# Kernel tuning notes

Hardware: AMD Instinct MI355X
Metric: run time of the kernel (lower is better)

The kernel has to match this reference:

```python
import jax, jax.numpy as jnp
import numpy as np

B, N, C = 32, 577, 768
H = 12
D = C // H
HID = 4 * C
EPS = 1e-5


def setup_inputs() -> dict:
    key = jax.random.key(0)
    ks = jax.random.split(key, 12)
    s = 0.02
    return {
        "x": jax.random.normal(ks[0], (B, N, C), dtype=jnp.float32),
        "ln1_g": jnp.ones((C,), jnp.float32),
        "ln1_b": jnp.zeros((C,), jnp.float32),
        "qkv_w": jax.random.normal(ks[1], (C, 3 * C), jnp.float32) * s,
        "qkv_b": jnp.zeros((3 * C,), jnp.float32),
        "proj_w": jax.random.normal(ks[2], (C, C), jnp.float32) * s,
        "proj_b": jnp.zeros((C,), jnp.float32),
        "ln2_g": jnp.ones((C,), jnp.float32),
        "ln2_b": jnp.zeros((C,), jnp.float32),
        "fc1_w": jax.random.normal(ks[3], (C, HID), jnp.float32) * s,
        "fc1_b": jnp.zeros((HID,), jnp.float32),
        "fc2_w": jax.random.normal(ks[4], (HID, C), jnp.float32) * s,
        "fc2_b": jnp.zeros((C,), jnp.float32),
    }


def _layernorm(x, g, b):
    mu = jnp.mean(x, axis=-1, keepdims=True)
    var = jnp.mean(jnp.square(x - mu), axis=-1, keepdims=True)
    return (x - mu) * jax.lax.rsqrt(var + EPS) * g + b


def reference(x, ln1_g, ln1_b, qkv_w, qkv_b, proj_w, proj_b,
              ln2_g, ln2_b, fc1_w, fc1_b, fc2_w, fc2_b):
    b, n, c = x.shape
    # --- MSA branch ---
    h = _layernorm(x, ln1_g, ln1_b)
    qkv = h @ qkv_w + qkv_b                      # [b, n, 3c]
    qkv = qkv.reshape(b, n, 3, H, D).transpose(2, 0, 3, 1, 4)  # [3, b, h, n, d]
    q, k, v = qkv[0], qkv[1], qkv[2]
    scale = D ** -0.5
    attn = jnp.einsum('bhqd,bhkd->bhqk', q, k) * scale
    attn = jax.nn.softmax(attn, axis=-1)
    o = jnp.einsum('bhqk,bhkd->bhqd', attn, v)   # [b, h, n, d]
    o = o.transpose(0, 2, 1, 3).reshape(b, n, c)
    o = o @ proj_w + proj_b
    x = x + o
    # --- MLP branch ---
    h = _layernorm(x, ln2_g, ln2_b)
    h = jax.nn.gelu(h @ fc1_w + fc1_b, approximate=False)  # torch nn.GELU = exact erf
    h = h @ fc2_w + fc2_b
    return x + h
```

## Files before the change

### kernel.cpp

```cpp
#include <hip/hip_runtime.h>

typedef unsigned short u16;
typedef short short8 __attribute__((ext_vector_type(8)));
typedef float f32x4 __attribute__((ext_vector_type(4)));

#define MM 18464
#define NTOK 577

__device__ __forceinline__ u16 f2bf(float f) {
    unsigned u = __builtin_bit_cast(unsigned, f);
    u += 0x7fffu + ((u >> 16) & 1u);
    return (u16)(u >> 16);
}

__device__ __forceinline__ void gload16(const void* g, void* lds) {
    __builtin_amdgcn_global_load_lds(
        (const __attribute__((address_space(1))) unsigned*)g,
        (__attribute__((address_space(3))) unsigned*)lds,
        16, 0, 0);
}

__device__ __forceinline__ int2 xcd_swz(int gx, int gy) {
    const int nwg = gx * gy;
    const int flat = blockIdx.x + blockIdx.y * gx;
    const int q = nwg >> 3, r = nwg & 7;
    const int xcd = flat & 7, lid = flat >> 3;
    const int w = (xcd < r ? xcd * (q + 1) : r * (q + 1) + (xcd - r) * q) + lid;
    int2 o; o.x = w % gx; o.y = w / gx; return o;
}

__global__ __launch_bounds__(256) void convT(const float* __restrict__ src,
                                             u16* __restrict__ dst, int K, int N) {
    __shared__ float tile[32][33];
    const int k0 = blockIdx.x * 32, n0 = blockIdx.y * 32;
    const int tx = threadIdx.x & 31, ty = threadIdx.x >> 5;
#pragma unroll
    for (int i = 0; i < 32; i += 8)
        tile[ty + i][tx] = src[(size_t)(k0 + ty + i) * N + n0 + tx];
    __syncthreads();
#pragma unroll
    for (int i = 0; i < 32; i += 8)
        dst[(size_t)(n0 + ty + i) * K + k0 + tx] = f2bf(tile[tx][ty + i]);
}

__global__ __launch_bounds__(192) void ln_k(const float* __restrict__ x,
                                            const float* __restrict__ g,
                                            const float* __restrict__ bt,
                                            u16* __restrict__ out) {
    const int row = blockIdx.x, t = threadIdx.x;
    const float4 v = reinterpret_cast<const float4*>(x + (size_t)row * 768)[t];
    float s = v.x + v.y + v.z + v.w;
    float s2 = v.x * v.x + v.y * v.y + v.z * v.z + v.w * v.w;
#pragma unroll
    for (int off = 32; off > 0; off >>= 1) {
        s += __shfl_down(s, off);
        s2 += __shfl_down(s2, off);
    }
    __shared__ float red[6];
    if ((t & 63) == 0) { red[t >> 6] = s; red[3 + (t >> 6)] = s2; }
    __syncthreads();
    const float S = red[0] + red[1] + red[2];
    const float S2 = red[3] + red[4] + red[5];
    const float mu = S * (1.f / 768.f);
    const float var = S2 * (1.f / 768.f) - mu * mu;
    const float rs = rsqrtf(var + 1e-5f);
    const float4 gg = reinterpret_cast<const float4*>(g)[t];
    const float4 bb = reinterpret_cast<const float4*>(bt)[t];
    ushort4 r;
    r.x = f2bf((v.x - mu) * rs * gg.x + bb.x);
    r.y = f2bf((v.y - mu) * rs * gg.y + bb.y);
    r.z = f2bf((v.z - mu) * rs * gg.z + bb.z);
    r.w = f2bf((v.w - mu) * rs * gg.w + bb.w);
    reinterpret_cast<ushort4*>(out + (size_t)row * 768)[t] = r;
}

template <int MODE>
__global__ __launch_bounds__(256) void gemm_k(const u16* __restrict__ A,
                                              const u16* __restrict__ BT,
                                              const float* __restrict__ bias,
                                              const float* __restrict__ resid,
                                              void* __restrict__ outp,
                                              int M, int N, int K) {
    __shared__ u16 As[2][128 * 32];
    __shared__ u16 Bs[2][128 * 32];
    const int t = threadIdx.x;
    const int wid = t >> 6, lane = t & 63;
    const int l15 = lane & 15, lg = lane >> 4;
    const int2 sw = xcd_swz(gridDim.x, gridDim.y);
    const int m0 = sw.x * 128, n0 = sw.y * 128;
    const int wr = wid >> 1, wc = wid & 1;

    f32x4 acc[4][4] = {};

    const int srow = t >> 2;
    const int sk = (t & 3) * 8;
    const size_t a0 = (size_t)min(m0 + srow, M - 1) * K + sk;
    const size_t a1 = (size_t)min(m0 + srow + 64, M - 1) * K + sk;
    const size_t b0 = (size_t)(n0 + srow) * K + sk;
    const size_t b1 = (size_t)(n0 + srow + 64) * K + sk;
    const int wo = wid * 512;

    auto stage = [&](int buf, int k0) {
        gload16(A + a0 + k0, &As[buf][wo]);
        gload16(A + a1 + k0, &As[buf][wo + 2048]);
        gload16(BT + b0 + k0, &Bs[buf][wo]);
        gload16(BT + b1 + k0, &Bs[buf][wo + 2048]);
    };
    auto compute = [&](int buf) {
        short8 af[4], bfr[4];
#pragma unroll
        for (int fr = 0; fr < 4; ++fr)
            af[fr] = *(const short8*)&As[buf][(wr * 64 + fr * 16 + l15) * 32 + lg * 8];
#pragma unroll
        for (int fc = 0; fc < 4; ++fc)
            bfr[fc] = *(const short8*)&Bs[buf][(wc * 64 + fc * 16 + l15) * 32 + lg * 8];
#pragma unroll
        for (int fr = 0; fr < 4; ++fr)
#pragma unroll
            for (int fc = 0; fc < 4; ++fc)
                acc[fr][fc] = __builtin_amdgcn_mfma_f32_16x16x32_bf16(
                    af[fr], bfr[fc], acc[fr][fc], 0, 0, 0);
    };

    stage(0, 0);
    __syncthreads();
    int cur = 0;
    const int nk = K >> 5;
    for (int kt = 1; kt < nk; ++kt) {
        stage(cur ^ 1, kt * 32);
        compute(cur);
        __syncthreads();
        cur ^= 1;
    }
    compute(cur);

    float bcol[4];
#pragma unroll
    for (int fc = 0; fc < 4; ++fc) bcol[fc] = bias[n0 + wc * 64 + fc * 16 + l15];
#pragma unroll
    for (int fr = 0; fr < 4; ++fr) {
#pragma unroll
        for (int reg = 0; reg < 4; ++reg) {
            const int row = m0 + wr * 64 + fr * 16 + lg * 4 + reg;
            if (row < M) {
#pragma unroll
                for (int fc = 0; fc < 4; ++fc) {
                    const int col = n0 + wc * 64 + fc * 16 + l15;
                    float v = acc[fr][fc][reg] + bcol[fc];
                    if (MODE == 2) v = 0.5f * v * (1.0f + erff(v * 0.70710678118f));
                    if (MODE == 1 || MODE == 3) v += resid[(size_t)row * N + col];
                    if (MODE == 0 || MODE == 2)
                        ((u16*)outp)[(size_t)row * N + col] = f2bf(v);
                    else
                        ((float*)outp)[(size_t)row * N + col] = v;
                }
            }
        }
    }
}

__global__ __launch_bounds__(256) void attn_k(const u16* __restrict__ qkv,
                                              u16* __restrict__ o) {
    const int2 sw = xcd_swz(10, 384);
    const int qt = sw.x;
    const int bh = sw.y;
    const int b = bh / 12, h = bh % 12;
    const int t = threadIdx.x, wid = t >> 6, lane = t & 63;
    const int l15 = lane & 15, lg = lane >> 4;
    const size_t base = ((size_t)b * NTOK) * 2304 + (size_t)h * 64;

    __shared__ u16 Ks[64 * 64], VT[64 * 64], Ps[64 * 64];

    int qrow = qt * 64 + wid * 16 + l15;
    qrow = min(qrow, NTOK - 1);
    const u16* Qp = qkv + base + (size_t)qrow * 2304 + lg * 8;
    const short8 qf0 = *(const short8*)(Qp);
    const short8 qf1 = *(const short8*)(Qp + 32);

    f32x4 oacc[4] = {};
    float m_run[4], l_run[4];
#pragma unroll
    for (int j = 0; j < 4; ++j) { m_run[j] = -1e30f; l_run[j] = 0.f; }

    const int srow = t >> 3;
    const int cchunk = t & 7;
    const int ksd = (cchunk ^ (srow & 7)) * 8;
    u16* ldsK = Ks + wid * 512;
    const int vs0 = ((srow >> 3) ^ cchunk) * 8 + (srow & 7);
    const int vs1 = (((srow >> 3) + 4) ^ cchunk) * 8 + (srow & 7);

    for (int kt = 0; kt < 10; ++kt) {
        const int n0t = kt * 64;
        const int r0 = min(n0t + srow, NTOK - 1);
        const int r1 = min(n0t + srow + 32, NTOK - 1);
        gload16(qkv + base + 768 + (size_t)r0 * 2304 + ksd, ldsK);
        gload16(qkv + base + 768 + (size_t)r1 * 2304 + ksd, ldsK + 2048);
        const short8 v0 = *(const short8*)(qkv + base + 1536 + (size_t)r0 * 2304 + cchunk * 8);
        const short8 v1 = *(const short8*)(qkv + base + 1536 + (size_t)r1 * 2304 + cchunk * 8);
#pragma unroll
        for (int j = 0; j < 8; ++j) {
            VT[(cchunk * 8 + j) * 64 + vs0] = (u16)v0[j];
            VT[(cchunk * 8 + j) * 64 + vs1] = (u16)v1[j];
        }
        __syncthreads();

        f32x4 s[4];
#pragma unroll
        for (int fc = 0; fc < 4; ++fc) {
            const int krow = fc * 16 + l15;
            const short8 kf0 = *(const short8*)&Ks[krow * 64 + ((lg ^ (krow & 7)) * 8)];
            const short8 kf1 = *(const short8*)&Ks[krow * 64 + (((lg + 4) ^ (krow & 7)) * 8)];
            f32x4 a_ = {};
            a_ = __builtin_amdgcn_mfma_f32_16x16x32_bf16(qf0, kf0, a_, 0, 0, 0);
            a_ = __builtin_amdgcn_mfma_f32_16x16x32_bf16(qf1, kf1, a_, 0, 0, 0);
            s[fc] = a_;
        }
#pragma unroll
        for (int fc = 0; fc < 4; ++fc) {
            const bool valid = (n0t + fc * 16 + l15) < NTOK;
#pragma unroll
            for (int j = 0; j < 4; ++j)
                s[fc][j] = valid ? s[fc][j] * 0.125f : -1e30f;
        }
        float mt[4];
#pragma unroll
        for (int j = 0; j < 4; ++j)
            mt[j] = fmaxf(fmaxf(s[0][j], s[1][j]), fmaxf(s[2][j], s[3][j]));
#pragma unroll
        for (int off = 1; off < 16; off <<= 1)
#pragma unroll
            for (int j = 0; j < 4; ++j) mt[j] = fmaxf(mt[j], __shfl_xor(mt[j], off));
        float mn[4], alpha[4];
#pragma unroll
        for (int j = 0; j < 4; ++j) {
            mn[j] = fmaxf(m_run[j], mt[j]);
            alpha[j] = __expf(m_run[j] - mn[j]);
            m_run[j] = mn[j];
        }
        float lsum[4] = {0.f, 0.f, 0.f, 0.f};
#pragma unroll
        for (int fc = 0; fc < 4; ++fc)
#pragma unroll
            for (int j = 0; j < 4; ++j) {
                const float p = __expf(s[fc][j] - mn[j]);
                s[fc][j] = p;
                lsum[j] += p;
            }
#pragma unroll
        for (int off = 1; off < 16; off <<= 1)
#pragma unroll
            for (int j = 0; j < 4; ++j) lsum[j] += __shfl_xor(lsum[j], off);
#pragma unroll
        for (int j = 0; j < 4; ++j) l_run[j] = l_run[j] * alpha[j] + lsum[j];
#pragma unroll
        for (int fc = 0; fc < 4; ++fc)
#pragma unroll
            for (int j = 0; j < 4; ++j) oacc[fc][j] *= alpha[j];

#pragma unroll
        for (int fc = 0; fc < 4; ++fc)
#pragma unroll
            for (int j = 0; j < 4; ++j) {
                const int q = wid * 16 + lg * 4 + j;
                Ps[q * 64 + (((fc * 2 + (l15 >> 3)) ^ (q & 7)) * 8) + (l15 & 7)] =
                    f2bf(s[fc][j]);
            }
        asm volatile("s_waitcnt lgkmcnt(0)" ::: "memory");

#pragma unroll
        for (int c = 0; c < 2; ++c) {
            const short8 pf = *(const short8*)
                &Ps[(wid * 16 + l15) * 64 + (((c * 4 + lg) ^ (l15 & 7)) * 8)];
#pragma unroll
            for (int fc = 0; fc < 4; ++fc) {
                const short8 vf = *(const short8*)
                    &VT[(fc * 16 + l15) * 64 +
                        (((c * 4 + lg) ^ (fc * 2 + (l15 >> 3))) * 8)];
                oacc[fc] = __builtin_amdgcn_mfma_f32_16x16x32_bf16(pf, vf, oacc[fc], 0, 0, 0);
            }
        }
        __syncthreads();
    }

#pragma unroll
    for (int j = 0; j < 4; ++j) {
        const int row = qt * 64 + wid * 16 + lg * 4 + j;
        if (row < NTOK) {
            const float inv = 1.0f / l_run[j];
#pragma unroll
            for (int fc = 0; fc < 4; ++fc)
                o[((size_t)(b * NTOK + row)) * 768 + h * 64 + fc * 16 + l15] =
                    f2bf(oacc[fc][j] * inv);
        }
    }
}

extern "C" void kernel_launch(void* const* d_in, const int* in_sizes, int n_in,
                              void* d_out, int out_size, void* d_ws, size_t ws_size,
                              hipStream_t stream) {
    const float* x      = (const float*)d_in[0];
    const float* ln1_g  = (const float*)d_in[1];
    const float* ln1_b  = (const float*)d_in[2];
    const float* qkv_w  = (const float*)d_in[3];
    const float* qkv_b  = (const float*)d_in[4];
    const float* proj_w = (const float*)d_in[5];
    const float* proj_b = (const float*)d_in[6];
    const float* ln2_g  = (const float*)d_in[7];
    const float* ln2_b  = (const float*)d_in[8];
    const float* fc1_w  = (const float*)d_in[9];
    const float* fc1_b  = (const float*)d_in[10];
    const float* fc2_w  = (const float*)d_in[11];
    const float* fc2_b  = (const float*)d_in[12];
    float* out = (float*)d_out;

    char* ws = (char*)d_ws;
    size_t off = 0;
    u16* WQ  = (u16*)(ws + off); off += (size_t)2304 * 768 * 2;
    u16* WP  = (u16*)(ws + off); off += (size_t)768 * 768 * 2;
    u16* W1  = (u16*)(ws + off); off += (size_t)3072 * 768 * 2;
    u16* W2  = (u16*)(ws + off); off += (size_t)768 * 3072 * 2;
    u16* LN1 = (u16*)(ws + off); off += (size_t)MM * 768 * 2;
    u16* QKV = (u16*)(ws + off); off += (size_t)MM * 2304 * 2;
    u16* OB  = (u16*)(ws + off); off += (size_t)MM * 768 * 2;
    float* X1 = (float*)(ws + off); off += (size_t)MM * 768 * 4;
    u16* LN2 = (u16*)(ws + off); off += (size_t)MM * 768 * 2;
    u16* HID = LN1;

    convT<<<dim3(24, 72), 256, 0, stream>>>(qkv_w, WQ, 768, 2304);
    convT<<<dim3(24, 24), 256, 0, stream>>>(proj_w, WP, 768, 768);
    convT<<<dim3(24, 96), 256, 0, stream>>>(fc1_w, W1, 768, 3072);
    convT<<<dim3(96, 24), 256, 0, stream>>>(fc2_w, W2, 3072, 768);

    ln_k<<<MM, 192, 0, stream>>>(x, ln1_g, ln1_b, LN1);
    gemm_k<0><<<dim3(145, 18), 256, 0, stream>>>(LN1, WQ, qkv_b, nullptr, QKV,
                                                 MM, 2304, 768);
    attn_k<<<dim3(10, 384), 256, 0, stream>>>(QKV, OB);
    gemm_k<1><<<dim3(145, 6), 256, 0, stream>>>(OB, WP, proj_b, x, X1,
                                                MM, 768, 768);
    ln_k<<<MM, 192, 0, stream>>>(X1, ln2_g, ln2_b, LN2);
    gemm_k<2><<<dim3(145, 24), 256, 0, stream>>>(LN2, W1, fc1_b, nullptr, HID,
                                                 MM, 3072, 768);
    gemm_k<3><<<dim3(145, 6), 256, 0, stream>>>(HID, W2, fc2_b, X1, out,
                                                MM, 768, 3072);
}
```

Measured before the change: 849.2 us.

## Move GEMMs to 256x256 tiles with swizzled LDS and a two-stage async pipeline

Rewrites the shared GEMM kernel to use 512-thread blocks computing 256x256 output tiles with a K-step of 64, so each staged byte is reused across more MFMAs. LDS tiles are XOR-swizzled to avoid bank conflicts on fragment reads. A two-deep global_load_lds prefetch is gated by explicit vmcnt waits and barriers, and the MFMA block is wrapped in s_setprio. The cost is 128 KB of LDS per block, which allows one block per CU. The narrow proj and fc2 GEMMs now launch fewer blocks than there are CUs, and the M tail wastes more work.

```diff
diff --git a/kernel.cpp b/kernel.cpp
--- a/kernel.cpp
+++ b/kernel.cpp
@@ -20,12 +20,14 @@
         16, 0, 0);
 }
 
-__device__ __forceinline__ int2 xcd_swz(int gx, int gy) {
-    const int nwg = gx * gy;
-    const int flat = blockIdx.x + blockIdx.y * gx;
+__device__ __forceinline__ int xcd_map(int flat, int nwg) {
     const int q = nwg >> 3, r = nwg & 7;
     const int xcd = flat & 7, lid = flat >> 3;
-    const int w = (xcd < r ? xcd * (q + 1) : r * (q + 1) + (xcd - r) * q) + lid;
+    return (xcd < r ? xcd * (q + 1) : r * (q + 1) + (xcd - r) * q) + lid;
+}
+
+__device__ __forceinline__ int2 xcd_swz2(int gx, int gy) {
+    const int w = xcd_map(blockIdx.x + blockIdx.y * gx, gx * gy);
     int2 o; o.x = w % gx; o.y = w / gx; return o;
 }
 
@@ -75,78 +77,93 @@
 }
 
 template <int MODE>
-__global__ __launch_bounds__(256) void gemm_k(const u16* __restrict__ A,
-                                              const u16* __restrict__ BT,
-                                              const float* __restrict__ bias,
-                                              const float* __restrict__ resid,
-                                              void* __restrict__ outp,
-                                              int M, int N, int K) {
-    __shared__ u16 As[2][128 * 32];
-    __shared__ u16 Bs[2][128 * 32];
+__global__ __launch_bounds__(512, 2) void gemm_k(const u16* __restrict__ A,
+                                                 const u16* __restrict__ BT,
+                                                 const float* __restrict__ bias,
+                                                 const float* __restrict__ resid,
+                                                 void* __restrict__ outp,
+                                                 int M, int N, int K, int mt) {
+    __shared__ u16 smem[4][256 * 64];
     const int t = threadIdx.x;
     const int wid = t >> 6, lane = t & 63;
     const int l15 = lane & 15, lg = lane >> 4;
-    const int2 sw = xcd_swz(gridDim.x, gridDim.y);
-    const int m0 = sw.x * 128, n0 = sw.y * 128;
-    const int wr = wid >> 1, wc = wid & 1;
-
-    f32x4 acc[4][4] = {};
-
-    const int srow = t >> 2;
-    const int sk = (t & 3) * 8;
-    const size_t a0 = (size_t)min(m0 + srow, M - 1) * K + sk;
-    const size_t a1 = (size_t)min(m0 + srow + 64, M - 1) * K + sk;
-    const size_t b0 = (size_t)(n0 + srow) * K + sk;
-    const size_t b1 = (size_t)(n0 + srow + 64) * K + sk;
-    const int wo = wid * 512;
+    const int wr = wid >> 2, wc = wid & 3;
+
+    const int w = xcd_map(blockIdx.x, gridDim.x);
+    const int m0 = (w % mt) * 256, n0 = (w / mt) * 256;
+
+    f32x4 acc[8][4] = {};
+    const int NT = K >> 6;
 
     auto stage = [&](int buf, int k0) {
-        gload16(A + a0 + k0, &As[buf][wo]);
-        gload16(A + a1 + k0, &As[buf][wo + 2048]);
-        gload16(BT + b0 + k0, &Bs[buf][wo]);
-        gload16(BT + b1 + k0, &Bs[buf][wo + 2048]);
+        u16* Ad = smem[buf * 2];
+        u16* Bd = smem[buf * 2 + 1];
+#pragma unroll
+        for (int i = 0; i < 4; ++i) {
+            const int slot = i * 512 + t;
+            const int r = slot >> 3, sl = slot & 7;
+            const int cs = (sl ^ (r & 7)) << 3;
+            const size_t dofs = (size_t)(i * 512 + (t & ~63)) * 8;
+            gload16(A + (size_t)min(m0 + r, M - 1) * K + k0 + cs, Ad + dofs);
+            gload16(BT + (size_t)(n0 + r) * K + k0 + cs, Bd + dofs);
+        }
     };
+
     auto compute = [&](int buf) {
-        short8 af[4], bfr[4];
-#pragma unroll
-        for (int fr = 0; fr < 4; ++fr)
-            af[fr] = *(const short8*)&As[buf][(wr * 64 + fr * 16 + l15) * 32 + lg * 8];
-#pragma unroll
-        for (int fc = 0; fc < 4; ++fc)
-            bfr[fc] = *(const short8*)&Bs[buf][(wc * 64 + fc * 16 + l15) * 32 + lg * 8];
-#pragma unroll
-        for (int fr = 0; fr < 4; ++fr)
-#pragma unroll
-            for (int fc = 0; fc < 4; ++fc)
-                acc[fr][fc] = __builtin_amdgcn_mfma_f32_16x16x32_bf16(
-                    af[fr], bfr[fc], acc[fr][fc], 0, 0, 0);
+        const u16* Ab = smem[buf * 2];
+        const u16* Bb = smem[buf * 2 + 1];
+#pragma unroll
+        for (int half = 0; half < 2; ++half) {
+            short8 af[8], bf4[4];
+#pragma unroll
+            for (int mf = 0; mf < 8; ++mf) {
+                const int r = wr * 128 + mf * 16 + l15;
+                af[mf] = *(const short8*)&Ab[r * 64 + (((half * 4 + lg) ^ (l15 & 7)) << 3)];
+            }
+#pragma unroll
+            for (int nf = 0; nf < 4; ++nf) {
+                const int r = wc * 64 + nf * 16 + l15;
+                bf4[nf] = *(const short8*)&Bb[r * 64 + (((half * 4 + lg) ^ (l15 & 7)) << 3)];
+            }
+            __builtin_amdgcn_s_setprio(1);
+#pragma unroll
+            for (int mf = 0; mf < 8; ++mf)
+#pragma unroll
+                for (int nf = 0; nf < 4; ++nf)
+                    acc[mf][nf] = __builtin_amdgcn_mfma_f32_16x16x32_bf16(
+                        af[mf], bf4[nf], acc[mf][nf], 0, 0, 0);
+            __builtin_amdgcn_s_setprio(0);
+        }
     };
 
     stage(0, 0);
-    __syncthreads();
-    int cur = 0;
-    const int nk = K >> 5;
-    for (int kt = 1; kt < nk; ++kt) {
-        stage(cur ^ 1, kt * 32);
-        compute(cur);
-        __syncthreads();
-        cur ^= 1;
-    }
-    compute(cur);
+    stage(1, 64);
+    for (int tt = 0; tt < NT; ++tt) {
+        if (tt < NT - 1) asm volatile("s_waitcnt vmcnt(8)" ::: "memory");
+        else             asm volatile("s_waitcnt vmcnt(0)" ::: "memory");
+        __builtin_amdgcn_s_barrier();
+        __builtin_amdgcn_sched_barrier(0);
+        compute(tt & 1);
+        __builtin_amdgcn_sched_barrier(0);
+        asm volatile("s_waitcnt lgkmcnt(0)" ::: "memory");
+        __builtin_amdgcn_s_barrier();
+        __builtin_amdgcn_sched_barrier(0);
+        if (tt + 2 < NT) stage(tt & 1, (tt + 2) << 6);
+    }
 
     float bcol[4];
 #pragma unroll
-    for (int fc = 0; fc < 4; ++fc) bcol[fc] = bias[n0 + wc * 64 + fc * 16 + l15];
-#pragma unroll
-    for (int fr = 0; fr < 4; ++fr) {
+    for (int nf = 0; nf < 4; ++nf) bcol[nf] = bias[n0 + wc * 64 + nf * 16 + l15];
+#pragma unroll
+    for (int mf = 0; mf < 8; ++mf) {
 #pragma unroll
         for (int reg = 0; reg < 4; ++reg) {
-            const int row = m0 + wr * 64 + fr * 16 + lg * 4 + reg;
+            const int row = m0 + wr * 128 + mf * 16 + lg * 4 + reg;
             if (row < M) {
 #pragma unroll
-                for (int fc = 0; fc < 4; ++fc) {
-                    const int col = n0 + wc * 64 + fc * 16 + l15;
-                    float v = acc[fr][fc][reg] + bcol[fc];
+                for (int nf = 0; nf < 4; ++nf) {
+                    const int col = n0 + wc * 64 + nf * 16 + l15;
+                    float v = acc[mf][nf][reg] + bcol[nf];
                     if (MODE == 2) v = 0.5f * v * (1.0f + erff(v * 0.70710678118f));
                     if (MODE == 1 || MODE == 3) v += resid[(size_t)row * N + col];
                     if (MODE == 0 || MODE == 2)
@@ -161,7 +178,7 @@
 
 __global__ __launch_bounds__(256) void attn_k(const u16* __restrict__ qkv,
                                               u16* __restrict__ o) {
-    const int2 sw = xcd_swz(10, 384);
+    const int2 sw = xcd_swz2(10, 384);
     const int qt = sw.x;
     const int bh = sw.y;
     const int b = bh / 12, h = bh % 12;
@@ -222,18 +239,18 @@
             for (int j = 0; j < 4; ++j)
                 s[fc][j] = valid ? s[fc][j] * 0.125f : -1e30f;
         }
-        float mt[4];
+        float mt_[4];
 #pragma unroll
         for (int j = 0; j < 4; ++j)
-            mt[j] = fmaxf(fmaxf(s[0][j], s[1][j]), fmaxf(s[2][j], s[3][j]));
+            mt_[j] = fmaxf(fmaxf(s[0][j], s[1][j]), fmaxf(s[2][j], s[3][j]));
 #pragma unroll
         for (int off = 1; off < 16; off <<= 1)
 #pragma unroll
-            for (int j = 0; j < 4; ++j) mt[j] = fmaxf(mt[j], __shfl_xor(mt[j], off));
+            for (int j = 0; j < 4; ++j) mt_[j] = fmaxf(mt_[j], __shfl_xor(mt_[j], off));
         float mn[4], alpha[4];
 #pragma unroll
         for (int j = 0; j < 4; ++j) {
-            mn[j] = fmaxf(m_run[j], mt[j]);
+            mn[j] = fmaxf(m_run[j], mt_[j]);
             alpha[j] = __expf(m_run[j] - mn[j]);
             m_run[j] = mn[j];
         }
@@ -331,15 +348,16 @@
     convT<<<dim3(24, 96), 256, 0, stream>>>(fc1_w, W1, 768, 3072);
     convT<<<dim3(96, 24), 256, 0, stream>>>(fc2_w, W2, 3072, 768);
 
+    const int mt = (MM + 255) / 256;
     ln_k<<<MM, 192, 0, stream>>>(x, ln1_g, ln1_b, LN1);
-    gemm_k<0><<<dim3(145, 18), 256, 0, stream>>>(LN1, WQ, qkv_b, nullptr, QKV,
-                                                 MM, 2304, 768);
+    gemm_k<0><<<mt * 9, 512, 0, stream>>>(LN1, WQ, qkv_b, nullptr, QKV,
+                                          MM, 2304, 768, mt);
     attn_k<<<dim3(10, 384), 256, 0, stream>>>(QKV, OB);
-    gemm_k<1><<<dim3(145, 6), 256, 0, stream>>>(OB, WP, proj_b, x, X1,
-                                                MM, 768, 768);
+    gemm_k<1><<<mt * 3, 512, 0, stream>>>(OB, WP, proj_b, x, X1,
+                                          MM, 768, 768, mt);
     ln_k<<<MM, 192, 0, stream>>>(X1, ln2_g, ln2_b, LN2);
-    gemm_k<2><<<dim3(145, 24), 256, 0, stream>>>(LN2, W1, fc1_b, nullptr, HID,
-                                                 MM, 3072, 768);
-    gemm_k<3><<<dim3(145, 6), 256, 0, stream>>>(HID, W2, fc2_b, X1, out,
-                                                MM, 768, 3072);
-}
+    gemm_k<2><<<mt * 12, 512, 0, stream>>>(LN2, W1, fc1_b, nullptr, HID,
+                                           MM, 3072, 768, mt);
+    gemm_k<3><<<mt * 3, 512, 0, stream>>>(HID, W2, fc2_b, X1, out,
+                                          MM, 768, 3072, mt);
+}
```

Result: faster. 749.6 us (-11.7%).
